# Kernel tuning notes

Hardware: AMD Instinct MI355X
Metric: run time of the kernel (lower is better)

The kernel has to match this reference:

```python
import jax, jax.numpy as jnp
import numpy as np

H, C = 3, 64          # heads, out_channels
NEG_SLOPE = 0.2       # PyG GATConv leaky_relu default
LN_EPS = 1e-5


def setup_inputs() -> dict:
    key = jax.random.key(0)
    ks = jax.random.split(key, 20)
    N, E, D_in, edge_dim = 50000, 800000, 64, 5
    g = lambda k, shape: (jax.random.normal(k, shape, dtype=jnp.float32) * 0.1)
    return {
        "x": jax.random.normal(ks[0], (N, D_in), dtype=jnp.float32),
        "edge_attr": jax.random.normal(ks[1], (E, edge_dim), dtype=jnp.float32),
        "lin_w": g(ks[2], (D_in, H * C)),          # GATConv.lin (bias=False)
        "att_src": g(ks[3], (H, C)),
        "att_dst": g(ks[4], (H, C)),
        "lin_edge_w": g(ks[5], (edge_dim, H * C)),  # GATConv.lin_edge (bias=False)
        "att_edge": g(ks[6], (H, C)),
        "gat_bias": jnp.zeros((H * C,), jnp.float32),
        "w1": g(ks[7], (H * C, C)),
        "b1": jnp.zeros((C,), jnp.float32),
        "ln1_g": jnp.ones((C,), jnp.float32),
        "ln1_b": jnp.zeros((C,), jnp.float32),
        "w2": g(ks[8], (C, C)),
        "b2": jnp.zeros((C,), jnp.float32),
        "ln2_g": jnp.ones((C,), jnp.float32),
        "ln2_b": jnp.zeros((C,), jnp.float32),
        "edge_index": jax.random.randint(ks[9], (2, E), 0, N),
    }


def layer_norm(x, g, b):
    m = jnp.mean(x, axis=-1, keepdims=True)
    v = jnp.mean((x - m) ** 2, axis=-1, keepdims=True)
    return (x - m) * jax.lax.rsqrt(v + LN_EPS) * g + b


def gat_conv(x, edge_index, edge_attr, lin_w, att_src, att_dst,
             lin_edge_w, att_edge, gat_bias):
    N = x.shape[0]
    src, dst = edge_index[0], edge_index[1]

    # add_self_loops=True with fill_value='mean': self-loop edge_attr is the
    # per-node mean of incoming edge attributes (0 if node has no in-edges).
    attr_sum = jax.ops.segment_sum(edge_attr, dst, num_segments=N)       # [N, edge_dim]
    cnt = jax.ops.segment_sum(jnp.ones((dst.shape[0],), edge_attr.dtype), dst, num_segments=N)
    loop_attr = attr_sum / jnp.maximum(cnt, 1.0)[:, None]
    loop = jnp.arange(N, dtype=src.dtype)
    src = jnp.concatenate([src, loop])
    dst = jnp.concatenate([dst, loop])
    ea = jnp.concatenate([edge_attr, loop_attr], axis=0)                  # [E2, edge_dim]

    xs = (x @ lin_w).reshape(N, H, C)                                     # [N, H, C]
    a_src = jnp.einsum('nhc,hc->nh', xs, att_src)                         # [N, H]
    a_dst = jnp.einsum('nhc,hc->nh', xs, att_dst)                         # [N, H]
    e = (ea @ lin_edge_w).reshape(-1, H, C)                               # [E2, H, C]
    a_edge = jnp.einsum('ehc,hc->eh', e, att_edge)                        # [E2, H]

    logits = a_src[src] + a_dst[dst] + a_edge                             # [E2, H]
    logits = jnp.where(logits >= 0, logits, NEG_SLOPE * logits)           # leaky_relu

    # segment softmax over incoming edges of each dst node (self loops ensure non-empty)
    lmax = jax.ops.segment_max(logits, dst, num_segments=N)               # [N, H]
    ex = jnp.exp(logits - lmax[dst])
    denom = jax.ops.segment_sum(ex, dst, num_segments=N)                  # [N, H]
    alpha = ex / denom[dst]                                               # [E2, H]

    msgs = alpha[:, :, None] * xs[src]                                    # [E2, H, C]
    out = jax.ops.segment_sum(msgs, dst, num_segments=N)                  # [N, H, C]
    return out.reshape(N, H * C) + gat_bias


def reference(x, edge_attr, lin_w, att_src, att_dst, lin_edge_w, att_edge,
              gat_bias, w1, b1, ln1_g, ln1_b, w2, b2, ln2_g, ln2_b, edge_index):
    x_gat = gat_conv(x, edge_index, edge_attr, lin_w, att_src, att_dst,
                     lin_edge_w, att_edge, gat_bias)
    x_gat = x_gat @ w1 + b1                         # linear1: [N, C]
    x_gat = layer_norm(x + x_gat, ln1_g, ln1_b)     # layerNorm1(x + x_gat)
    lin = x_gat @ w2 + b2                           # linear2
    out = layer_norm(lin + x_gat, ln2_g, ln2_b)     # layerNorm2(lin + x_gat)
    return out                                      # dropout p=0 -> identity
```

## Files before the change

### kernel.cpp

```cpp
#include <hip/hip_runtime.h>


#define HH 3
#define CC 64
#define DIN 64
#define ED 5
#define HC 192
#define NEG_SLOPE 0.2f
#define LN_EPS 1e-5f

typedef __attribute__((ext_vector_type(8))) short bf16x8;
typedef __attribute__((ext_vector_type(4))) float f32x4;

__device__ __forceinline__ float leaky(float l) { return (l >= 0.f) ? l : NEG_SLOPE * l; }

__device__ __forceinline__ unsigned short f2bf(float f) {
    unsigned u = __float_as_uint(f);
    unsigned r = (u + 0x7FFFu + ((u >> 16) & 1u)) >> 16;
    return (unsigned short)r;
}
__device__ __forceinline__ float bf2f(unsigned short u) {
    return __uint_as_float((unsigned)u << 16);
}

__device__ __forceinline__ bf16x8 pack8(float4 a, float4 b) {
    bf16x8 r;
    r[0] = (short)f2bf(a.x); r[1] = (short)f2bf(a.y);
    r[2] = (short)f2bf(a.z); r[3] = (short)f2bf(a.w);
    r[4] = (short)f2bf(b.x); r[5] = (short)f2bf(b.y);
    r[6] = (short)f2bf(b.z); r[7] = (short)f2bf(b.w);
    return r;
}

#define PREP_TOT (HC*DIN + DIN*HC + CC*CC + CC + ED*HH)
#define PREP_BLOCKS 30
__global__ __launch_bounds__(256) void k_prep_cnt(const float* __restrict__ lin_w,
                                                  const float* __restrict__ w1,
                                                  const float* __restrict__ w2,
                                                  const float* __restrict__ b1,
                                                  const float* __restrict__ gat_bias,
                                                  const float* __restrict__ lin_edge_w,
                                                  const float* __restrict__ att_edge,
                                                  unsigned short* __restrict__ linwt,
                                                  unsigned short* __restrict__ w1t,
                                                  unsigned short* __restrict__ w2t,
                                                  float* __restrict__ b1p,
                                                  float* __restrict__ we,
                                                  const int* __restrict__ ei,
                                                  int* __restrict__ icnt, int E) {
    if (blockIdx.x < PREP_BLOCKS) {
        for (int i = blockIdx.x * 256 + threadIdx.x; i < PREP_TOT; i += PREP_BLOCKS * 256) {
            if (i < HC * DIN) {
                int c = i >> 6, k = i & 63;
                linwt[i] = f2bf(lin_w[k * HC + c]);
            } else if (i < 2 * HC * DIN) {
                int j = i - HC * DIN;
                int c = j / HC, k = j - c * HC;
                w1t[j] = f2bf(w1[k * CC + c]);
            } else if (i < 2 * HC * DIN + CC * CC) {
                int j = i - 2 * HC * DIN;
                int c = j >> 6, k = j & 63;
                w2t[j] = f2bf(w2[k * CC + c]);
            } else if (i < 2 * HC * DIN + CC * CC + CC) {
                int c = i - (2 * HC * DIN + CC * CC);
                float s = b1[c];
                for (int k = 0; k < HC; ++k) s += gat_bias[k] * w1[k * CC + c];
                b1p[c] = s;
            } else {
                int q = i - (2 * HC * DIN + CC * CC + CC);
                int d = q / HH, h = q - d * HH;
                float s = 0.f;
                for (int c = 0; c < CC; ++c)
                    s += lin_edge_w[d * HC + h * CC + c] * att_edge[h * CC + c];
                we[q] = s;
            }
        }
    } else {
        int nb = gridDim.x - PREP_BLOCKS;
        for (int e = (blockIdx.x - PREP_BLOCKS) * 256 + threadIdx.x; e < E; e += nb * 256)
            atomicAdd(&icnt[ei[E + e]], 1);
    }
}

__global__ __launch_bounds__(256) void k_xs(const float* __restrict__ x,
                                            const unsigned short* __restrict__ linwt,
                                            const float* __restrict__ att_src,
                                            const float* __restrict__ att_dst,
                                            unsigned short* __restrict__ xsb,
                                            float* __restrict__ a_src,
                                            float* __restrict__ a_dst, int N) {
    int lane = threadIdx.x & 63, w = threadIdx.x >> 6;
    int l15 = lane & 15, kg = (lane >> 4) * 8;
    int nb = blockIdx.x * 64;
    int arow = nb + w * 16 + l15;
    int arow_c = min(arow, N - 1);

    f32x4 acc[12];
    #pragma unroll
    for (int ct = 0; ct < 12; ++ct) acc[ct] = (f32x4){0.f, 0.f, 0.f, 0.f};

    #pragma unroll
    for (int k0 = 0; k0 < DIN; k0 += 32) {
        const float* ap = x + (size_t)arow_c * DIN + k0 + kg;
        float4 a0 = *(const float4*)ap;
        float4 a1 = *(const float4*)(ap + 4);
        bf16x8 af = pack8(a0, a1);
        #pragma unroll
        for (int ct = 0; ct < 12; ++ct) {
            bf16x8 bf = *(const bf16x8*)(linwt + (size_t)(ct * 16 + l15) * DIN + k0 + kg);
            acc[ct] = __builtin_amdgcn_mfma_f32_16x16x32_bf16(af, bf, acc[ct], 0, 0, 0);
        }
    }

    float asv[12], adv[12];
    #pragma unroll
    for (int ct = 0; ct < 12; ++ct) {
        int c = ct * 16 + l15;
        asv[ct] = att_src[c]; adv[ct] = att_dst[c];
    }

    int rbase = nb + w * 16 + (lane >> 4) * 4;
    #pragma unroll
    for (int j = 0; j < 4; ++j) {
        int r = rbase + j;
        bool ok = r < N;
        float ps0 = 0.f, ps1 = 0.f, ps2 = 0.f, pd0 = 0.f, pd1 = 0.f, pd2 = 0.f;
        #pragma unroll
        for (int ct = 0; ct < 12; ++ct) {
            float v = acc[ct][j];
            if (ok) xsb[(size_t)r * HC + ct * 16 + l15] = f2bf(v);
            float s = v * asv[ct], d = v * adv[ct];
            if (ct < 4)      { ps0 += s; pd0 += d; }
            else if (ct < 8) { ps1 += s; pd1 += d; }
            else             { ps2 += s; pd2 += d; }
        }
        #pragma unroll
        for (int o = 1; o < 16; o <<= 1) {
            ps0 += __shfl_xor(ps0, o, 64); pd0 += __shfl_xor(pd0, o, 64);
            ps1 += __shfl_xor(ps1, o, 64); pd1 += __shfl_xor(pd1, o, 64);
            ps2 += __shfl_xor(ps2, o, 64); pd2 += __shfl_xor(pd2, o, 64);
        }
        if (ok && l15 == 0) {
            a_src[r * HH + 0] = ps0; a_src[r * HH + 1] = ps1; a_src[r * HH + 2] = ps2;
            a_dst[r * HH + 0] = pd0; a_dst[r * HH + 1] = pd1; a_dst[r * HH + 2] = pd2;
        }
    }
}

__global__ __launch_bounds__(256) void k_scan1(const int* __restrict__ icnt,
                                               int* __restrict__ bsum, int N) {
    int i = blockIdx.x * 256 + threadIdx.x;
    int lane = threadIdx.x & 63, wid = threadIdx.x >> 6;
    int v = (i < N) ? icnt[i] : 0;
    #pragma unroll
    for (int o = 32; o; o >>= 1) v += __shfl_xor(v, o, 64);
    __shared__ int wt[4];
    if (lane == 0) wt[wid] = v;
    __syncthreads();
    if (threadIdx.x == 0) bsum[blockIdx.x] = wt[0] + wt[1] + wt[2] + wt[3];
}

__global__ __launch_bounds__(1024) void k_scan2(const int* __restrict__ bsum,
                                                int* __restrict__ boff, int nb) {
    __shared__ int s[1024];
    int t = threadIdx.x;
    int v = (t < nb) ? bsum[t] : 0;
    s[t] = v;
    __syncthreads();
    for (int d = 1; d < 1024; d <<= 1) {
        int u = (t >= d) ? s[t - d] : 0;
        __syncthreads();
        s[t] += u;
        __syncthreads();
    }
    if (t < nb) boff[t] = s[t] - v;
}

__global__ __launch_bounds__(256) void k_scan3(const int* __restrict__ icnt,
                                               const int* __restrict__ boff,
                                               int* __restrict__ off,
                                               int* __restrict__ cursor, int N) {
    int i = blockIdx.x * 256 + threadIdx.x;
    int lane = threadIdx.x & 63, wid = threadIdx.x >> 6;
    int v = (i < N) ? icnt[i] : 0;
    int incl = v;
    #pragma unroll
    for (int o = 1; o < 64; o <<= 1) {
        int u = __shfl_up(incl, o, 64);
        if (lane >= o) incl += u;
    }
    __shared__ int wt[4];
    if (lane == 63) wt[wid] = incl;
    __syncthreads();
    int wpre = 0;
    for (int w = 0; w < wid; ++w) wpre += wt[w];
    int excl = boff[blockIdx.x] + wpre + incl - v;
    if (i < N) {
        off[i] = excl;
        cursor[i] = excl;
        if (i == N - 1) off[N] = excl + v;
    }
}

__global__ __launch_bounds__(256) void k_fill(const float* __restrict__ ea,
                                              const int* __restrict__ ei,
                                              const float* __restrict__ a_src,
                                              const float* __restrict__ we,
                                              int* __restrict__ cursor,
                                              uint4* __restrict__ payload, int E) {
    int e = blockIdx.x * blockDim.x + threadIdx.x;
    if (e >= E) return;
    int s = ei[e], d = ei[E + e];
    float attr[ED];
    #pragma unroll
    for (int j = 0; j < ED; ++j) attr[j] = ea[(size_t)e * ED + j];
    float aeh[HH], lp[HH];
    #pragma unroll
    for (int h = 0; h < HH; ++h) {
        float a = 0.f;
        #pragma unroll
        for (int j = 0; j < ED; ++j) a += attr[j] * we[j * HH + h];
        aeh[h] = a;
        lp[h] = a_src[s * HH + h] + a;
    }
    int pos = atomicAdd(&cursor[d], 1);
    uint4 pk;
    pk.x = (unsigned)f2bf(lp[0])  | ((unsigned)f2bf(lp[1])  << 16);
    pk.y = (unsigned)f2bf(lp[2])  | ((unsigned)f2bf(aeh[0]) << 16);
    pk.z = (unsigned)f2bf(aeh[1]) | ((unsigned)f2bf(aeh[2]) << 16);
    pk.w = (unsigned)s;
    payload[pos] = pk;
}

__global__ __launch_bounds__(256) void k_gat(const unsigned short* __restrict__ xsb,
                                             const float* __restrict__ a_src,
                                             const float* __restrict__ a_dst,
                                             const int* __restrict__ off,
                                             const uint4* __restrict__ payload,
                                             unsigned short* __restrict__ oaccb, int N) {
    __shared__ float4 wbuf[4][64];
    int lane = threadIdx.x & 63;
    int wid  = threadIdx.x >> 6;
    for (int n = blockIdx.x * 4 + wid; n < N; n += gridDim.x * 4) {
        int beg = off[n], end = off[n + 1];
        int deg = end - beg;
        float ad0 = a_dst[n * HH + 0], ad1 = a_dst[n * HH + 1], ad2 = a_dst[n * HH + 2];
        float pden0 = 0.f, pden1 = 0.f, pden2 = 0.f;
        float pae0 = 0.f, pae1 = 0.f, pae2 = 0.f;
        float acc0 = 0.f, acc1 = 0.f, acc2 = 0.f;

        for (int c0 = 0; c0 < deg; c0 += 64) {
            int cn = min(deg - c0, 64);
            float w0 = 0.f, w1 = 0.f, w2 = 0.f;
            int src = 0;
            if (lane < cn) {
                uint4 p = payload[beg + c0 + lane];
                float lp0 = bf2f((unsigned short)(p.x & 0xFFFFu)) + ad0;
                float lp1 = bf2f((unsigned short)(p.x >> 16)) + ad1;
                float lp2 = bf2f((unsigned short)(p.y & 0xFFFFu)) + ad2;
                w0 = __expf(leaky(lp0));
                w1 = __expf(leaky(lp1));
                w2 = __expf(leaky(lp2));
                pae0 += bf2f((unsigned short)(p.y >> 16));
                pae1 += bf2f((unsigned short)(p.z & 0xFFFFu));
                pae2 += bf2f((unsigned short)(p.z >> 16));
                pden0 += w0; pden1 += w1; pden2 += w2;
                src = (int)p.w;
            }
            wbuf[wid][lane] = make_float4(w0, w1, w2, __int_as_float(src));
            int i = 0;
            for (; i + 2 <= cn; i += 2) {
                float4 ta = wbuf[wid][i];
                float4 tb = wbuf[wid][i + 1];
                size_t sa = (size_t)__float_as_int(ta.w) * HC;
                size_t sb = (size_t)__float_as_int(tb.w) * HC;
                float xa0 = bf2f(xsb[sa + 0 * CC + lane]);
                float xa1 = bf2f(xsb[sa + 1 * CC + lane]);
                float xa2 = bf2f(xsb[sa + 2 * CC + lane]);
                float xb0 = bf2f(xsb[sb + 0 * CC + lane]);
                float xb1 = bf2f(xsb[sb + 1 * CC + lane]);
                float xb2 = bf2f(xsb[sb + 2 * CC + lane]);
                acc0 += ta.x * xa0; acc1 += ta.y * xa1; acc2 += ta.z * xa2;
                acc0 += tb.x * xb0; acc1 += tb.y * xb1; acc2 += tb.z * xb2;
            }
            if (i < cn) {
                float4 ta = wbuf[wid][i];
                size_t sa = (size_t)__float_as_int(ta.w) * HC;
                acc0 += ta.x * bf2f(xsb[sa + 0 * CC + lane]);
                acc1 += ta.y * bf2f(xsb[sa + 1 * CC + lane]);
                acc2 += ta.z * bf2f(xsb[sa + 2 * CC + lane]);
            }
        }

        #pragma unroll
        for (int o = 32; o; o >>= 1) {
            pden0 += __shfl_xor(pden0, o, 64);
            pden1 += __shfl_xor(pden1, o, 64);
            pden2 += __shfl_xor(pden2, o, 64);
            pae0  += __shfl_xor(pae0, o, 64);
            pae1  += __shfl_xor(pae1, o, 64);
            pae2  += __shfl_xor(pae2, o, 64);
        }

        float dc = fmaxf((float)deg, 1.0f);
        float sl0 = leaky(a_src[n * HH + 0] + ad0 + pae0 / dc);
        float sl1 = leaky(a_src[n * HH + 1] + ad1 + pae1 / dc);
        float sl2 = leaky(a_src[n * HH + 2] + ad2 + pae2 / dc);
        float e0 = __expf(sl0), e1 = __expf(sl1), e2 = __expf(sl2);
        size_t nbse = (size_t)n * HC;
        float den0 = pden0 + e0, den1 = pden1 + e1, den2 = pden2 + e2;
        acc0 += e0 * bf2f(xsb[nbse + 0 * CC + lane]);
        acc1 += e1 * bf2f(xsb[nbse + 1 * CC + lane]);
        acc2 += e2 * bf2f(xsb[nbse + 2 * CC + lane]);
        oaccb[nbse + 0 * CC + lane] = f2bf(acc0 / den0);
        oaccb[nbse + 1 * CC + lane] = f2bf(acc1 / den1);
        oaccb[nbse + 2 * CC + lane] = f2bf(acc2 / den2);
    }
}

__global__ __launch_bounds__(256) void k_mlp(const unsigned short* __restrict__ oaccb,
                                             const unsigned short* __restrict__ w1t,
                                             const unsigned short* __restrict__ w2t,
                                             const float* __restrict__ b1p,
                                             const float* __restrict__ x,
                                             const float* __restrict__ g1,
                                             const float* __restrict__ be1,
                                             const float* __restrict__ b2,
                                             const float* __restrict__ g2,
                                             const float* __restrict__ be2,
                                             float* __restrict__ out, int N) {
    __shared__ unsigned short H1[64 * 72];
    int lane = threadIdx.x & 63, w = threadIdx.x >> 6;
    int l15 = lane & 15, kg = (lane >> 4) * 8;
    int nb = blockIdx.x * 64;
    int arow = nb + w * 16 + l15;
    int arow_c = min(arow, N - 1);

    float c_b1[4], c_g1[4], c_be1[4], c_b2[4], c_g2[4], c_be2[4];
    #pragma unroll
    for (int ct = 0; ct < 4; ++ct) {
        int c = ct * 16 + l15;
        c_b1[ct] = b1p[c]; c_g1[ct] = g1[c]; c_be1[ct] = be1[c];
        c_b2[ct] = b2[c];  c_g2[ct] = g2[c]; c_be2[ct] = be2[c];
    }

    f32x4 acc[4];
    #pragma unroll
    for (int ct = 0; ct < 4; ++ct) acc[ct] = (f32x4){0.f, 0.f, 0.f, 0.f};
    #pragma unroll
    for (int k0 = 0; k0 < HC; k0 += 32) {
        bf16x8 af = *(const bf16x8*)(oaccb + (size_t)arow_c * HC + k0 + kg);
        #pragma unroll
        for (int ct = 0; ct < 4; ++ct) {
            bf16x8 bf = *(const bf16x8*)(w1t + (size_t)(ct * 16 + l15) * HC + k0 + kg);
            acc[ct] = __builtin_amdgcn_mfma_f32_16x16x32_bf16(af, bf, acc[ct], 0, 0, 0);
        }
    }

    int rbase = nb + w * 16 + (lane >> 4) * 4;
    int rloc0 = w * 16 + (lane >> 4) * 4;
    float h1v[4][4];
    float y[4][4];
    #pragma unroll
    for (int j = 0; j < 4; ++j) {
        int r = min(rbase + j, N - 1);
        #pragma unroll
        for (int ct = 0; ct < 4; ++ct)
            y[ct][j] = acc[ct][j] + c_b1[ct] + x[(size_t)r * DIN + ct * 16 + l15];
    }
    #pragma unroll
    for (int j = 0; j < 4; ++j) {
        float s = y[0][j] + y[1][j] + y[2][j] + y[3][j];
        #pragma unroll
        for (int o = 1; o < 16; o <<= 1) s += __shfl_xor(s, o, 64);
        float m = s * (1.0f / CC);
        float vs = 0.f;
        #pragma unroll
        for (int ct = 0; ct < 4; ++ct) { float d = y[ct][j] - m; vs += d * d; }
        #pragma unroll
        for (int o = 1; o < 16; o <<= 1) vs += __shfl_xor(vs, o, 64);
        float inv = rsqrtf(vs * (1.0f / CC) + LN_EPS);
        #pragma unroll
        for (int ct = 0; ct < 4; ++ct) {
            float h = (y[ct][j] - m) * inv * c_g1[ct] + c_be1[ct];
            h1v[ct][j] = h;
            H1[(rloc0 + j) * 72 + ct * 16 + l15] = f2bf(h);
        }
    }
    __syncthreads();

    f32x4 acc2[4];
    #pragma unroll
    for (int ct = 0; ct < 4; ++ct) acc2[ct] = (f32x4){0.f, 0.f, 0.f, 0.f};
    #pragma unroll
    for (int k0 = 0; k0 < CC; k0 += 32) {
        bf16x8 af = *(const bf16x8*)&H1[(w * 16 + l15) * 72 + k0 + kg];
        #pragma unroll
        for (int ct = 0; ct < 4; ++ct) {
            bf16x8 bf = *(const bf16x8*)(w2t + (size_t)(ct * 16 + l15) * CC + k0 + kg);
            acc2[ct] = __builtin_amdgcn_mfma_f32_16x16x32_bf16(af, bf, acc2[ct], 0, 0, 0);
        }
    }

    #pragma unroll
    for (int j = 0; j < 4; ++j) {
        float z0 = acc2[0][j] + c_b2[0] + h1v[0][j];
        float z1 = acc2[1][j] + c_b2[1] + h1v[1][j];
        float z2 = acc2[2][j] + c_b2[2] + h1v[2][j];
        float z3 = acc2[3][j] + c_b2[3] + h1v[3][j];
        float s = z0 + z1 + z2 + z3;
        #pragma unroll
        for (int o = 1; o < 16; o <<= 1) s += __shfl_xor(s, o, 64);
        float m = s * (1.0f / CC);
        float d0 = z0 - m, d1 = z1 - m, d2 = z2 - m, d3 = z3 - m;
        float vs = d0 * d0 + d1 * d1 + d2 * d2 + d3 * d3;
        #pragma unroll
        for (int o = 1; o < 16; o <<= 1) vs += __shfl_xor(vs, o, 64);
        float inv = rsqrtf(vs * (1.0f / CC) + LN_EPS);
        int r = rbase + j;
        if (r < N) {
            out[(size_t)r * CC + 0 * 16 + l15] = d0 * inv * c_g2[0] + c_be2[0];
            out[(size_t)r * CC + 1 * 16 + l15] = d1 * inv * c_g2[1] + c_be2[1];
            out[(size_t)r * CC + 2 * 16 + l15] = d2 * inv * c_g2[2] + c_be2[2];
            out[(size_t)r * CC + 3 * 16 + l15] = d3 * inv * c_g2[3] + c_be2[3];
        }
    }
}

extern "C" void kernel_launch(void* const* d_in, const int* in_sizes, int n_in,
                              void* d_out, int out_size, void* d_ws, size_t ws_size,
                              hipStream_t stream) {
    const float* x          = (const float*)d_in[0];
    const float* edge_attr  = (const float*)d_in[1];
    const float* lin_w      = (const float*)d_in[2];
    const float* att_src    = (const float*)d_in[3];
    const float* att_dst    = (const float*)d_in[4];
    const float* lin_edge_w = (const float*)d_in[5];
    const float* att_edge   = (const float*)d_in[6];
    const float* gat_bias   = (const float*)d_in[7];
    const float* w1         = (const float*)d_in[8];
    const float* b1         = (const float*)d_in[9];
    const float* ln1_g      = (const float*)d_in[10];
    const float* ln1_b      = (const float*)d_in[11];
    const float* w2         = (const float*)d_in[12];
    const float* b2         = (const float*)d_in[13];
    const float* ln2_g      = (const float*)d_in[14];
    const float* ln2_b      = (const float*)d_in[15];
    const int*   ei         = (const int*)d_in[16];
    float* out = (float*)d_out;

    const int N = in_sizes[0] / DIN;
    const int E = in_sizes[1] / ED;
    const int nb_scan = (N + 255) / 256;

    char* ws = (char*)d_ws;
    size_t off_b = 0;
    auto alloc = [&](size_t bytes) {
        size_t o = off_b;
        off_b = (off_b + bytes + 255) & ~(size_t)255;
        return o;
    };
    int* icnt = (int*)(ws + alloc((size_t)N * 4));
    size_t zero_bytes = off_b;
    unsigned short* xsb   = (unsigned short*)(ws + alloc((size_t)N * HC * 2));
    unsigned short* oaccb = (unsigned short*)(ws + alloc((size_t)N * HC * 2));
    float*  a_srcb  = (float*)(ws + alloc((size_t)N * HH * 4));
    float*  a_dstb  = (float*)(ws + alloc((size_t)N * HH * 4));
    int*    offb    = (int*)(ws + alloc((size_t)(N + 1) * 4));
    int*    cursor  = (int*)(ws + alloc((size_t)N * 4));
    int*    bsum    = (int*)(ws + alloc((size_t)nb_scan * 4));
    int*    boff    = (int*)(ws + alloc((size_t)nb_scan * 4));
    uint4*  payload = (uint4*)(ws + alloc((size_t)E * 16));
    unsigned short* linwt = (unsigned short*)(ws + alloc((size_t)HC * DIN * 2));
    unsigned short* w1t   = (unsigned short*)(ws + alloc((size_t)DIN * HC * 2));
    unsigned short* w2t   = (unsigned short*)(ws + alloc((size_t)CC * CC * 2));
    float* b1p = (float*)(ws + alloc((size_t)CC * 4));
    float* we  = (float*)(ws + alloc((size_t)ED * HH * 4));
    (void)ws_size; (void)n_in; (void)out_size;

    hipMemsetAsync(d_ws, 0, zero_bytes, stream);

    k_prep_cnt<<<PREP_BLOCKS + (E + 255) / 256, 256, 0, stream>>>(
        lin_w, w1, w2, b1, gat_bias, lin_edge_w, att_edge,
        linwt, w1t, w2t, b1p, we, ei, icnt, E);
    k_xs<<<(N + 63) / 64, 256, 0, stream>>>(x, linwt, att_src, att_dst, xsb, a_srcb, a_dstb, N);
    k_scan1<<<nb_scan, 256, 0, stream>>>(icnt, bsum, N);
    k_scan2<<<1, 1024, 0, stream>>>(bsum, boff, nb_scan);
    k_scan3<<<nb_scan, 256, 0, stream>>>(icnt, boff, offb, cursor, N);
    k_fill<<<(E + 255) / 256, 256, 0, stream>>>(edge_attr, ei, a_srcb, we, cursor,
                                                payload, E);
    k_gat<<<(N + 3) / 4, 256, 0, stream>>>(xsb, a_srcb, a_dstb, offb, payload, oaccb, N);
    k_mlp<<<(N + 63) / 64, 256, 0, stream>>>(oaccb, w1t, w2t, b1p, x,
                                             ln1_g, ln1_b, b2, ln2_g, ln2_b, out, N);
}
```

Measured before the change: 196.8 us.

## Interleave head features per channel and shrink CSR edge payload to 8 bytes

Stores the projected node features interleaved so each lane gathers its three head values with one 8-byte load instead of three 2-byte loads. The per-edge CSR payload shrinks from 16 to 8 bytes by packing a 16-bit source index beside the bf16 logits. A fallback int array handles node counts above 65536. Edge-attention sums for the self-loop mean move to atomics in the fill kernel, and log2e is folded into the logits so exp2f can be used. This cuts gather and payload traffic in the aggregation kernel, at the cost of three float atomics per edge.

```diff
diff --git a/kernel.cpp b/kernel.cpp
--- a/kernel.cpp
+++ b/kernel.cpp
@@ -8,6 +8,7 @@
 #define HC 192
 #define NEG_SLOPE 0.2f
 #define LN_EPS 1e-5f
+#define LOG2E 1.44269504f
 
 typedef __attribute__((ext_vector_type(8))) short bf16x8;
 typedef __attribute__((ext_vector_type(4))) float f32x4;
@@ -19,8 +20,11 @@
     unsigned r = (u + 0x7FFFu + ((u >> 16) & 1u)) >> 16;
     return (unsigned short)r;
 }
-__device__ __forceinline__ float bf2f(unsigned short u) {
-    return __uint_as_float((unsigned)u << 16);
+__device__ __forceinline__ float bf_lo(unsigned v) {
+    return __uint_as_float(v << 16);
+}
+__device__ __forceinline__ float bf_hi(unsigned v) {
+    return __uint_as_float(v & 0xFFFF0000u);
 }
 
 __device__ __forceinline__ bf16x8 pack8(float4 a, float4 b) {
@@ -72,7 +76,7 @@
                 float s = 0.f;
                 for (int c = 0; c < CC; ++c)
                     s += lin_edge_w[d * HC + h * CC + c] * att_edge[h * CC + c];
-                we[q] = s;
+                we[q] = s * LOG2E;
             }
         }
     } else {
@@ -86,7 +90,7 @@
                                             const unsigned short* __restrict__ linwt,
                                             const float* __restrict__ att_src,
                                             const float* __restrict__ att_dst,
-                                            unsigned short* __restrict__ xsb,
+                                            uint2* __restrict__ xsp,
                                             float* __restrict__ a_src,
                                             float* __restrict__ a_dst, int N) {
     int lane = threadIdx.x & 63, w = threadIdx.x >> 6;
@@ -128,12 +132,20 @@
         #pragma unroll
         for (int ct = 0; ct < 12; ++ct) {
             float v = acc[ct][j];
-            if (ok) xsb[(size_t)r * HC + ct * 16 + l15] = f2bf(v);
             float s = v * asv[ct], d = v * adv[ct];
             if (ct < 4)      { ps0 += s; pd0 += d; }
             else if (ct < 8) { ps1 += s; pd1 += d; }
             else             { ps2 += s; pd2 += d; }
         }
+        if (ok) {
+            #pragma unroll
+            for (int ct = 0; ct < 4; ++ct) {
+                uint2 pk;
+                pk.x = (unsigned)f2bf(acc[ct][j]) | ((unsigned)f2bf(acc[ct + 4][j]) << 16);
+                pk.y = (unsigned)f2bf(acc[ct + 8][j]);
+                xsp[(size_t)r * CC + ct * 16 + l15] = pk;
+            }
+        }
         #pragma unroll
         for (int o = 1; o < 16; o <<= 1) {
             ps0 += __shfl_xor(ps0, o, 64); pd0 += __shfl_xor(pd0, o, 64);
@@ -141,8 +153,10 @@
             ps2 += __shfl_xor(ps2, o, 64); pd2 += __shfl_xor(pd2, o, 64);
         }
         if (ok && l15 == 0) {
-            a_src[r * HH + 0] = ps0; a_src[r * HH + 1] = ps1; a_src[r * HH + 2] = ps2;
-            a_dst[r * HH + 0] = pd0; a_dst[r * HH + 1] = pd1; a_dst[r * HH + 2] = pd2;
+            a_src[r * HH + 0] = ps0 * LOG2E; a_src[r * HH + 1] = ps1 * LOG2E;
+            a_src[r * HH + 2] = ps2 * LOG2E;
+            a_dst[r * HH + 0] = pd0 * LOG2E; a_dst[r * HH + 1] = pd1 * LOG2E;
+            a_dst[r * HH + 2] = pd2 * LOG2E;
         }
     }
 }
@@ -207,7 +221,10 @@
                                               const float* __restrict__ a_src,
                                               const float* __restrict__ we,
                                               int* __restrict__ cursor,
-                                              uint4* __restrict__ payload, int E) {
+                                              uint2* __restrict__ payload,
+                                              int* __restrict__ srcext,
+                                              float* __restrict__ aesum,
+                                              int E, int use_ext) {
     int e = blockIdx.x * blockDim.x + threadIdx.x;
     if (e >= E) return;
     int s = ei[e], d = ei[E + e];
@@ -223,21 +240,26 @@
         aeh[h] = a;
         lp[h] = a_src[s * HH + h] + a;
     }
+    atomicAdd(&aesum[d * HH + 0], aeh[0]);
+    atomicAdd(&aesum[d * HH + 1], aeh[1]);
+    atomicAdd(&aesum[d * HH + 2], aeh[2]);
     int pos = atomicAdd(&cursor[d], 1);
-    uint4 pk;
-    pk.x = (unsigned)f2bf(lp[0])  | ((unsigned)f2bf(lp[1])  << 16);
-    pk.y = (unsigned)f2bf(lp[2])  | ((unsigned)f2bf(aeh[0]) << 16);
-    pk.z = (unsigned)f2bf(aeh[1]) | ((unsigned)f2bf(aeh[2]) << 16);
-    pk.w = (unsigned)s;
+    uint2 pk;
+    pk.x = (unsigned)f2bf(lp[0]) | ((unsigned)f2bf(lp[1]) << 16);
+    pk.y = (unsigned)f2bf(lp[2]) | ((unsigned)s << 16);
     payload[pos] = pk;
-}
-
-__global__ __launch_bounds__(256) void k_gat(const unsigned short* __restrict__ xsb,
+    if (use_ext) srcext[pos] = s;
+}
+
+__global__ __launch_bounds__(256) void k_gat(const uint2* __restrict__ xsp,
                                              const float* __restrict__ a_src,
                                              const float* __restrict__ a_dst,
+                                             const float* __restrict__ aesum,
                                              const int* __restrict__ off,
-                                             const uint4* __restrict__ payload,
-                                             unsigned short* __restrict__ oaccb, int N) {
+                                             const uint2* __restrict__ payload,
+                                             const int* __restrict__ srcext,
+                                             unsigned short* __restrict__ oaccb,
+                                             int N, int use_ext) {
     __shared__ float4 wbuf[4][64];
     int lane = threadIdx.x & 63;
     int wid  = threadIdx.x >> 6;
@@ -246,49 +268,39 @@
         int deg = end - beg;
         float ad0 = a_dst[n * HH + 0], ad1 = a_dst[n * HH + 1], ad2 = a_dst[n * HH + 2];
         float pden0 = 0.f, pden1 = 0.f, pden2 = 0.f;
-        float pae0 = 0.f, pae1 = 0.f, pae2 = 0.f;
-        float acc0 = 0.f, acc1 = 0.f, acc2 = 0.f;
+        float a0A = 0.f, a1A = 0.f, a2A = 0.f;
+        float a0B = 0.f, a1B = 0.f, a2B = 0.f;
 
         for (int c0 = 0; c0 < deg; c0 += 64) {
             int cn = min(deg - c0, 64);
             float w0 = 0.f, w1 = 0.f, w2 = 0.f;
             int src = 0;
             if (lane < cn) {
-                uint4 p = payload[beg + c0 + lane];
-                float lp0 = bf2f((unsigned short)(p.x & 0xFFFFu)) + ad0;
-                float lp1 = bf2f((unsigned short)(p.x >> 16)) + ad1;
-                float lp2 = bf2f((unsigned short)(p.y & 0xFFFFu)) + ad2;
-                w0 = __expf(leaky(lp0));
-                w1 = __expf(leaky(lp1));
-                w2 = __expf(leaky(lp2));
-                pae0 += bf2f((unsigned short)(p.y >> 16));
-                pae1 += bf2f((unsigned short)(p.z & 0xFFFFu));
-                pae2 += bf2f((unsigned short)(p.z >> 16));
+                uint2 p = payload[beg + c0 + lane];
+                w0 = exp2f(leaky(bf_lo(p.x) + ad0));
+                w1 = exp2f(leaky(bf_hi(p.x) + ad1));
+                w2 = exp2f(leaky(bf_lo(p.y) + ad2));
+                src = (int)(p.y >> 16);
+                if (use_ext) src = srcext[beg + c0 + lane];
                 pden0 += w0; pden1 += w1; pden2 += w2;
-                src = (int)p.w;
             }
             wbuf[wid][lane] = make_float4(w0, w1, w2, __int_as_float(src));
             int i = 0;
             for (; i + 2 <= cn; i += 2) {
                 float4 ta = wbuf[wid][i];
                 float4 tb = wbuf[wid][i + 1];
-                size_t sa = (size_t)__float_as_int(ta.w) * HC;
-                size_t sb = (size_t)__float_as_int(tb.w) * HC;
-                float xa0 = bf2f(xsb[sa + 0 * CC + lane]);
-                float xa1 = bf2f(xsb[sa + 1 * CC + lane]);
-                float xa2 = bf2f(xsb[sa + 2 * CC + lane]);
-                float xb0 = bf2f(xsb[sb + 0 * CC + lane]);
-                float xb1 = bf2f(xsb[sb + 1 * CC + lane]);
-                float xb2 = bf2f(xsb[sb + 2 * CC + lane]);
-                acc0 += ta.x * xa0; acc1 += ta.y * xa1; acc2 += ta.z * xa2;
-                acc0 += tb.x * xb0; acc1 += tb.y * xb1; acc2 += tb.z * xb2;
+                unsigned ia = (unsigned)__float_as_int(ta.w) * CC + lane;
+                unsigned ib = (unsigned)__float_as_int(tb.w) * CC + lane;
+                uint2 va = xsp[ia];
+                uint2 vb = xsp[ib];
+                a0A += ta.x * bf_lo(va.x); a1A += ta.y * bf_hi(va.x); a2A += ta.z * bf_lo(va.y);
+                a0B += tb.x * bf_lo(vb.x); a1B += tb.y * bf_hi(vb.x); a2B += tb.z * bf_lo(vb.y);
             }
             if (i < cn) {
                 float4 ta = wbuf[wid][i];
-                size_t sa = (size_t)__float_as_int(ta.w) * HC;
-                acc0 += ta.x * bf2f(xsb[sa + 0 * CC + lane]);
-                acc1 += ta.y * bf2f(xsb[sa + 1 * CC + lane]);
-                acc2 += ta.z * bf2f(xsb[sa + 2 * CC + lane]);
+                unsigned ia = (unsigned)__float_as_int(ta.w) * CC + lane;
+                uint2 va = xsp[ia];
+                a0A += ta.x * bf_lo(va.x); a1A += ta.y * bf_hi(va.x); a2A += ta.z * bf_lo(va.y);
             }
         }
 
@@ -297,21 +309,20 @@
             pden0 += __shfl_xor(pden0, o, 64);
             pden1 += __shfl_xor(pden1, o, 64);
             pden2 += __shfl_xor(pden2, o, 64);
-            pae0  += __shfl_xor(pae0, o, 64);
-            pae1  += __shfl_xor(pae1, o, 64);
-            pae2  += __shfl_xor(pae2, o, 64);
         }
 
         float dc = fmaxf((float)deg, 1.0f);
-        float sl0 = leaky(a_src[n * HH + 0] + ad0 + pae0 / dc);
-        float sl1 = leaky(a_src[n * HH + 1] + ad1 + pae1 / dc);
-        float sl2 = leaky(a_src[n * HH + 2] + ad2 + pae2 / dc);
-        float e0 = __expf(sl0), e1 = __expf(sl1), e2 = __expf(sl2);
+        float inv_dc = 1.0f / dc;
+        float sl0 = leaky(a_src[n * HH + 0] + ad0 + aesum[n * HH + 0] * inv_dc);
+        float sl1 = leaky(a_src[n * HH + 1] + ad1 + aesum[n * HH + 1] * inv_dc);
+        float sl2 = leaky(a_src[n * HH + 2] + ad2 + aesum[n * HH + 2] * inv_dc);
+        float e0 = exp2f(sl0), e1 = exp2f(sl1), e2 = exp2f(sl2);
+        uint2 vn = xsp[(unsigned)n * CC + lane];
+        float den0 = pden0 + e0, den1 = pden1 + e1, den2 = pden2 + e2;
+        float acc0 = a0A + a0B + e0 * bf_lo(vn.x);
+        float acc1 = a1A + a1B + e1 * bf_hi(vn.x);
+        float acc2 = a2A + a2B + e2 * bf_lo(vn.y);
         size_t nbse = (size_t)n * HC;
-        float den0 = pden0 + e0, den1 = pden1 + e1, den2 = pden2 + e2;
-        acc0 += e0 * bf2f(xsb[nbse + 0 * CC + lane]);
-        acc1 += e1 * bf2f(xsb[nbse + 1 * CC + lane]);
-        acc2 += e2 * bf2f(xsb[nbse + 2 * CC + lane]);
         oaccb[nbse + 0 * CC + lane] = f2bf(acc0 / den0);
         oaccb[nbse + 1 * CC + lane] = f2bf(acc1 / den1);
         oaccb[nbse + 2 * CC + lane] = f2bf(acc2 / den2);
@@ -452,6 +463,7 @@
     const int N = in_sizes[0] / DIN;
     const int E = in_sizes[1] / ED;
     const int nb_scan = (N + 255) / 256;
+    const int use_ext = (N > 65536) ? 1 : 0;
 
     char* ws = (char*)d_ws;
     size_t off_b = 0;
@@ -460,9 +472,10 @@
         off_b = (off_b + bytes + 255) & ~(size_t)255;
         return o;
     };
-    int* icnt = (int*)(ws + alloc((size_t)N * 4));
+    int*   icnt  = (int*)(ws + alloc((size_t)N * 4));
+    float* aesum = (float*)(ws + alloc((size_t)N * HH * 4));
     size_t zero_bytes = off_b;
-    unsigned short* xsb   = (unsigned short*)(ws + alloc((size_t)N * HC * 2));
+    uint2* xsp            = (uint2*)(ws + alloc((size_t)N * CC * 8));
     unsigned short* oaccb = (unsigned short*)(ws + alloc((size_t)N * HC * 2));
     float*  a_srcb  = (float*)(ws + alloc((size_t)N * HH * 4));
     float*  a_dstb  = (float*)(ws + alloc((size_t)N * HH * 4));
@@ -470,7 +483,8 @@
     int*    cursor  = (int*)(ws + alloc((size_t)N * 4));
     int*    bsum    = (int*)(ws + alloc((size_t)nb_scan * 4));
     int*    boff    = (int*)(ws + alloc((size_t)nb_scan * 4));
-    uint4*  payload = (uint4*)(ws + alloc((size_t)E * 16));
+    uint2*  payload = (uint2*)(ws + alloc((size_t)E * 8));
+    int*    srcext  = (int*)(ws + alloc((size_t)E * 4));
     unsigned short* linwt = (unsigned short*)(ws + alloc((size_t)HC * DIN * 2));
     unsigned short* w1t   = (unsigned short*)(ws + alloc((size_t)DIN * HC * 2));
     unsigned short* w2t   = (unsigned short*)(ws + alloc((size_t)CC * CC * 2));
@@ -483,13 +497,14 @@
     k_prep_cnt<<<PREP_BLOCKS + (E + 255) / 256, 256, 0, stream>>>(
         lin_w, w1, w2, b1, gat_bias, lin_edge_w, att_edge,
         linwt, w1t, w2t, b1p, we, ei, icnt, E);
-    k_xs<<<(N + 63) / 64, 256, 0, stream>>>(x, linwt, att_src, att_dst, xsb, a_srcb, a_dstb, N);
+    k_xs<<<(N + 63) / 64, 256, 0, stream>>>(x, linwt, att_src, att_dst, xsp, a_srcb, a_dstb, N);
     k_scan1<<<nb_scan, 256, 0, stream>>>(icnt, bsum, N);
     k_scan2<<<1, 1024, 0, stream>>>(bsum, boff, nb_scan);
     k_scan3<<<nb_scan, 256, 0, stream>>>(icnt, boff, offb, cursor, N);
     k_fill<<<(E + 255) / 256, 256, 0, stream>>>(edge_attr, ei, a_srcb, we, cursor,
-                                                payload, E);
-    k_gat<<<(N + 3) / 4, 256, 0, stream>>>(xsb, a_srcb, a_dstb, offb, payload, oaccb, N);
+                                                payload, srcext, aesum, E, use_ext);
+    k_gat<<<(N + 3) / 4, 256, 0, stream>>>(xsp, a_srcb, a_dstb, aesum, offb, payload,
+                                           srcext, oaccb, N, use_ext);
     k_mlp<<<(N + 63) / 64, 256, 0, stream>>>(oaccb, w1t, w2t, b1p, x,
                                              ln1_g, ln1_b, b2, ln2_g, ln2_b, out, N);
 }
```

Measured after the change: 311.8 us. 58.5% more time.
